# Optimization experiments

Hardware: AMD Instinct MI355X
Metric: run time of the kernel (lower is better)

The kernel has to match this reference:

```python
import jax, jax.numpy as jnp
import numpy as np

N_RAYS = 262144
N_SAMPLES = 128
NEAR, FAR = 0.0, 1.0
FAR_DELTA = 1e10  # sentinel delta for last sample


def setup_inputs() -> dict:
    key = jax.random.key(0)
    k1, k2, k3 = jax.random.split(key, 3)
    rgb = jax.random.uniform(k1, (N_RAYS, N_SAMPLES, 3), dtype=jnp.float32)
    density = jax.random.uniform(k2, (N_RAYS, N_SAMPLES, 1), dtype=jnp.float32)
    # distances must be increasing along sample axis, in [near, far]
    t = jax.random.uniform(k3, (N_RAYS, N_SAMPLES), dtype=jnp.float32)
    distances = NEAR + (FAR - NEAR) * jnp.sort(t, axis=-1)
    return {"rgb": rgb, "density": density, "distances": distances}


def reference(rgb, density, distances):
    # delta_i = t_{i+1} - t_i, last delta = 1e10
    delta = jnp.concatenate(
        [distances[..., 1:] - distances[..., :-1],
         jnp.full_like(distances[..., :1], FAR_DELTA)], axis=-1)
    alpha = 1.0 - jnp.exp(-density[..., 0] * delta)          # [N, S]
    # exclusive cumprod of (1 - alpha) -> transmittance
    transmittance = jnp.cumprod(
        jnp.concatenate([jnp.ones_like(alpha[..., :1]), 1.0 - alpha[..., :-1]], axis=-1),
        axis=-1)
    weights = alpha * transmittance                           # [N, S]
    rendered_rgb = jnp.sum(weights[..., None] * rgb, axis=-2)  # [N, 3]
    return rendered_rgb
```

## Files before the change

kernel.cpp:

```cpp
#include <hip/hip_runtime.h>


#define FAR_DELTA 1e10f

__global__ __launch_bounds__(256) void volrender_kernel(
    const float* __restrict__ rgb,
    const float* __restrict__ density,
    const float* __restrict__ dist,
    float* __restrict__ out,
    int n_rays)
{
    const int lane = threadIdx.x & 63;
    const int ray  = (blockIdx.x * blockDim.x + threadIdx.x) >> 6;
    if (ray >= n_rays) return;

    const size_t base128 = (size_t)ray * 128;
    const float2* d2 = (const float2*)(dist    + base128);
    const float2* s2 = (const float2*)(density + base128);
    const float2* c2 = (const float2*)(rgb + (size_t)ray * 384 + 6 * lane);

    float2 dd = d2[lane];
    float2 ss = s2[lane];

    float dnext  = __shfl_down(dd.x, 1);
    float delta0 = dd.y - dd.x;
    float delta1 = (lane == 63) ? FAR_DELTA : (dnext - dd.y);

    float x0 = ss.x * delta0;
    float x1 = ss.y * delta1;

    float x1s = (lane == 63) ? 0.0f : x1;
    float s   = x0 + x1s;

    float scan = s;
    #pragma unroll
    for (int off = 1; off < 64; off <<= 1) {
        float t = __shfl_up(scan, off);
        if (lane >= off) scan += t;
    }
    float cbase = scan - s;
    float c0 = cbase + x0;
    float c1 = c0 + x1;

    float T0 = __expf(-cbase);
    float T1 = __expf(-c0);
    float T2 = __expf(-c1);
    float w0 = T0 - T1;
    float w1 = T1 - T2;

    float2 r0 = c2[0];
    float2 r1 = c2[1];
    float2 r2 = c2[2];

    float accR = w0 * r0.x + w1 * r1.y;
    float accG = w0 * r0.y + w1 * r2.x;
    float accB = w0 * r1.x + w1 * r2.y;

    #pragma unroll
    for (int off = 32; off; off >>= 1) {
        accR += __shfl_down(accR, off);
        accG += __shfl_down(accG, off);
        accB += __shfl_down(accB, off);
    }

    if (lane == 0) {
        float* o = out + (size_t)ray * 3;
        o[0] = accR;
        o[1] = accG;
        o[2] = accB;
    }
}

extern "C" void kernel_launch(void* const* d_in, const int* in_sizes, int n_in,
                              void* d_out, int out_size, void* d_ws, size_t ws_size,
                              hipStream_t stream) {
    const float* rgb     = (const float*)d_in[0];
    const float* density = (const float*)d_in[1];
    const float* dist    = (const float*)d_in[2];
    float* out = (float*)d_out;

    const int n_rays = in_sizes[2] / 128;

    const int block = 256;
    const int rays_per_block = block / 64;
    const int grid = (n_rays + rays_per_block - 1) / rays_per_block;

    volrender_kernel<<<grid, block, 0, stream>>>(rgb, density, dist, out, n_rays);
}
```

Baseline: 651.7 us.

## Map one ray per thread with LDS-staged tiles and sequential transmittance

Replaces the one-wavefront-per-ray layout (shuffle scan plus shuffle reduction) with one thread per ray. Each 64-thread block stages 8-sample tiles of density, distance and rgb through shared memory and accumulates transmittance serially. This removes the cross-lane scan and reduction shuffles, at the cost of 16 barrier-separated tile loops per block, small blocks, and a serial dependency chain per thread.

After: 735.7 us. 12.9% more time.

```diff
diff --git a/kernel.cpp b/kernel.cpp
--- a/kernel.cpp
+++ b/kernel.cpp
@@ -3,68 +3,88 @@
 
 #define FAR_DELTA 1e10f
 
-__global__ __launch_bounds__(256) void volrender_kernel(
+__global__ __launch_bounds__(64) void volrender_kernel(
     const float* __restrict__ rgb,
     const float* __restrict__ density,
     const float* __restrict__ dist,
     float* __restrict__ out,
     int n_rays)
 {
-    const int lane = threadIdx.x & 63;
-    const int ray  = (blockIdx.x * blockDim.x + threadIdx.x) >> 6;
-    if (ray >= n_rays) return;
+    const int t  = threadIdx.x;
+    const int r0 = blockIdx.x << 6;
 
-    const size_t base128 = (size_t)ray * 128;
-    const float2* d2 = (const float2*)(dist    + base128);
-    const float2* s2 = (const float2*)(density + base128);
-    const float2* c2 = (const float2*)(rgb + (size_t)ray * 384 + 6 * lane);
+    __shared__ float SIG[64 * 12];
+    __shared__ float DST[64 * 12];
+    __shared__ float RGBT[64 * 28];
 
-    float2 dd = d2[lane];
-    float2 ss = s2[lane];
+    const int    ray  = min(r0 + t, n_rays - 1);
+    const size_t rowD = (size_t)ray * 128;
 
-    float dnext  = __shfl_down(dd.x, 1);
-    float delta0 = dd.y - dd.x;
-    float delta1 = (lane == 63) ? FAR_DELTA : (dnext - dd.y);
+    float T    = 1.0f;
+    float accR = 0.0f, accG = 0.0f, accB = 0.0f;
 
-    float x0 = ss.x * delta0;
-    float x1 = ss.y * delta1;
+    for (int tile = 0; tile < 16; ++tile) {
+        const int s0 = tile << 3;
 
-    float x1s = (lane == 63) ? 0.0f : x1;
-    float s   = x0 + x1s;
+        #pragma unroll
+        for (int k = 0; k < 2; ++k) {
+            const int    j   = t + (k << 6);
+            const int    row = j >> 1;
+            const int    col = (j & 1) << 2;
+            const int    gr  = min(r0 + row, n_rays - 1);
+            const size_t g   = (size_t)gr * 128 + s0 + col;
+            const float4 sv  = *(const float4*)(density + g);
+            const float4 dv  = *(const float4*)(dist + g);
+            *(float4*)(&SIG[row * 12 + col]) = sv;
+            *(float4*)(&DST[row * 12 + col]) = dv;
+        }
+        #pragma unroll
+        for (int k = 0; k < 6; ++k) {
+            const int    j   = t + (k << 6);
+            const int    row = j / 6;
+            const int    col = (j - row * 6) << 2;
+            const int    gr  = min(r0 + row, n_rays - 1);
+            const size_t g   = (size_t)gr * 384 + (size_t)s0 * 3 + col;
+            *(float4*)(&RGBT[row * 28 + col]) = *(const float4*)(rgb + g);
+        }
+        const float d_carry = dist[rowD + min(s0 + 8, 127)];
 
-    float scan = s;
-    #pragma unroll
-    for (int off = 1; off < 64; off <<= 1) {
-        float t = __shfl_up(scan, off);
-        if (lane >= off) scan += t;
-    }
-    float cbase = scan - s;
-    float c0 = cbase + x0;
-    float c1 = c0 + x1;
+        __syncthreads();
 
-    float T0 = __expf(-cbase);
-    float T1 = __expf(-c0);
-    float T2 = __expf(-c1);
-    float w0 = T0 - T1;
-    float w1 = T1 - T2;
+        const float4 sg0 = *(const float4*)(&SIG[t * 12]);
+        const float4 sg1 = *(const float4*)(&SIG[t * 12 + 4]);
+        const float4 dv0 = *(const float4*)(&DST[t * 12]);
+        const float4 dv1 = *(const float4*)(&DST[t * 12 + 4]);
 
-    float2 r0 = c2[0];
-    float2 r1 = c2[1];
-    float2 r2 = c2[2];
+        float cf[24];
+        #pragma unroll
+        for (int k = 0; k < 6; ++k) {
+            const float4 v = *(const float4*)(&RGBT[t * 28 + (k << 2)]);
+            cf[(k << 2) + 0] = v.x;  cf[(k << 2) + 1] = v.y;
+            cf[(k << 2) + 2] = v.z;  cf[(k << 2) + 3] = v.w;
+        }
 
-    float accR = w0 * r0.x + w1 * r1.y;
-    float accG = w0 * r0.y + w1 * r2.x;
-    float accB = w0 * r1.x + w1 * r2.y;
+        const float dl[9] = {dv0.x, dv0.y, dv0.z, dv0.w,
+                             dv1.x, dv1.y, dv1.z, dv1.w, d_carry};
+        const float sl[8] = {sg0.x, sg0.y, sg0.z, sg0.w,
+                             sg1.x, sg1.y, sg1.z, sg1.w};
 
-    #pragma unroll
-    for (int off = 32; off; off >>= 1) {
-        accR += __shfl_down(accR, off);
-        accG += __shfl_down(accG, off);
-        accB += __shfl_down(accB, off);
+        #pragma unroll
+        for (int j = 0; j < 8; ++j) {
+            const float delta = (s0 + j == 127) ? FAR_DELTA : (dl[j + 1] - dl[j]);
+            const float e = __expf(-sl[j] * delta);
+            const float w = T - T * e;
+            T *= e;
+            accR += w * cf[3 * j + 0];
+            accG += w * cf[3 * j + 1];
+            accB += w * cf[3 * j + 2];
+        }
+
+        __syncthreads();
     }
 
-    if (lane == 0) {
-        float* o = out + (size_t)ray * 3;
+    if (r0 + t < n_rays) {
+        float* o = out + (size_t)(r0 + t) * 3;
         o[0] = accR;
         o[1] = accG;
         o[2] = accB;
@@ -81,9 +101,8 @@
 
     const int n_rays = in_sizes[2] / 128;
 
-    const int block = 256;
-    const int rays_per_block = block / 64;
-    const int grid = (n_rays + rays_per_block - 1) / rays_per_block;
+    const int block = 64;
+    const int grid  = (n_rays + 63) / 64;
 
     volrender_kernel<<<grid, block, 0, stream>>>(rgb, density, dist, out, n_rays);
 }
```
